# Performance work log

Hardware: AMD Instinct MI355X
Metric: run time of the kernel (lower is better)

The kernel has to match this reference:

```python
import jax, jax.numpy as jnp
import numpy as np

NUM_EMBEDDINGS = 512
EMBEDDING_DIM = 64
COMMITMENT_COST = 0.25


def setup_inputs() -> dict:
    key = jax.random.key(0)
    k1, k2 = jax.random.split(key)
    inputs = jax.random.normal(k1, (64, 32, 32, EMBEDDING_DIM), dtype=jnp.float32)
    # nn.Embedding weight init: uniform(-1/K, 1/K)
    codebook = jax.random.uniform(
        k2, (NUM_EMBEDDINGS, EMBEDDING_DIM), dtype=jnp.float32,
        minval=-1.0 / NUM_EMBEDDINGS, maxval=1.0 / NUM_EMBEDDINGS)
    return {"inputs": inputs, "codebook": codebook}


def reference(inputs, codebook):
    D = codebook.shape[1]
    K = codebook.shape[0]
    flat = inputs.reshape(-1, D)  # [N, D]
    # Squared euclidean distances (argmin-equivalent to torch.cdist output)
    d2 = (jnp.sum(flat * flat, axis=1, keepdims=True)
          - 2.0 * (flat @ codebook.T)
          + jnp.sum(codebook * codebook, axis=1))  # [N, K]
    idx = jnp.argmin(d2, axis=1)  # [N]
    # Gather codebook rows (== one-hot @ codebook in the original)
    quantized = codebook[idx].reshape(inputs.shape)
    e_latent_loss = jnp.mean((jax.lax.stop_gradient(quantized) - inputs) ** 2)
    q_latent_loss = jnp.mean((quantized - jax.lax.stop_gradient(inputs)) ** 2)
    loss = q_latent_loss + COMMITMENT_COST * e_latent_loss
    # Straight-through estimator
    quantized_st = inputs + jax.lax.stop_gradient(quantized - inputs)
    # Perplexity from code usage histogram (== mean of one-hot encodings)
    n = flat.shape[0]
    avg_probs = jnp.zeros((K,), dtype=jnp.float32).at[idx].add(1.0) / n
    perplexity = jnp.exp(-jnp.sum(avg_probs * jnp.log(avg_probs + 1e-10)))
    encoding_indices = idx[:, None]  # [N, 1] to match torch unsqueeze(1)
    return (loss, quantized_st, perplexity, encoding_indices)
```

## Files before the change

### kernel.cpp

```cpp
#include <hip/hip_runtime.h>
#include <math.h>

#define K_EMB 512
#define DIM 64
#define NVEC 65536
#define OUT_LOSS 0
#define OUT_Q 1
#define OUT_PERP (1 + NVEC * DIM)
#define OUT_IDX (1 + NVEC * DIM + 1)
#define EPS2 1e-4f
#define FIX_CAP 16

typedef __attribute__((ext_vector_type(8))) short short8;
typedef __attribute__((ext_vector_type(4))) float float4v;


__device__ __forceinline__ unsigned short bf16_rn(float f) {
    unsigned u = __float_as_uint(f);
    return (unsigned short)((u + 0x7FFFu + ((u >> 16) & 1u)) >> 16);
}

__device__ __forceinline__ float np_pairwise8_sq(const float* v) {
    float r[8];
#pragma unroll
    for (int j = 0; j < 8; ++j) r[j] = __fmul_rn(v[j], v[j]);
#pragma unroll
    for (int i = 8; i < 64; i += 8) {
#pragma unroll
        for (int j = 0; j < 8; ++j) r[j] = __fadd_rn(r[j], __fmul_rn(v[i + j], v[i + j]));
    }
    return __fadd_rn(__fadd_rn(__fadd_rn(r[0], r[1]), __fadd_rn(r[2], r[3])),
                     __fadd_rn(__fadd_rn(r[4], r[5]), __fadd_rn(r[6], r[7])));
}

__global__ void vq_frag(const float* __restrict__ codebook, float* __restrict__ csq,
                        unsigned short* __restrict__ ahi, unsigned short* __restrict__ alo,
                        float4* __restrict__ csqf, unsigned* __restrict__ hist,
                        double* __restrict__ sse64) {
    const int tid = threadIdx.x;
    if (blockIdx.x < 16) {
        const int id = blockIdx.x * 256 + tid;
        const int t = id >> 7, step = (id >> 6) & 1, lane = id & 63;
        const int m = t * 16 + (lane & 15);
        const int kb = step * 32 + (lane >> 4) * 8;
        const float4* src = (const float4*)(codebook + (m << 6) + kb);
        float4 f0 = src[0], f1 = src[1];
        const float fs[8] = {f0.x, f0.y, f0.z, f0.w, f1.x, f1.y, f1.z, f1.w};
        short8 h, l;
#pragma unroll
        for (int j = 0; j < 8; ++j) {
            unsigned short hv = bf16_rn(fs[j]);
            float lof = fs[j] - __uint_as_float(((unsigned)hv) << 16);
            h[j] = (short)hv;
            l[j] = (short)bf16_rn(lof);
        }
        const int fo = ((t * 2 + step) * 64 + lane) * 8;
        *(short8*)(ahi + fo) = h;
        *(short8*)(alo + fo) = l;
    } else {
        __shared__ float s_csq[512];
#pragma unroll
        for (int r = 0; r < 2; ++r) {
            const int k = tid + 256 * r;
            float v = np_pairwise8_sq(codebook + ((size_t)k << 6));
            s_csq[k] = v;
            csq[k] = v;
            hist[k] = 0u;
        }
        if (tid < 64) sse64[tid] = 0.0;
        __syncthreads();
#pragma unroll
        for (int i = 0; i < 8; ++i) {
            const int id = i * 256 + tid;
            const int t = id >> 6, lane = id & 63;
            const int k0 = t * 16 + (lane >> 4) * 4;
            csqf[id] = make_float4(s_csq[k0], s_csq[k0 + 1], s_csq[k0 + 2], s_csq[k0 + 3]);
        }
    }
}

__launch_bounds__(256, 4)
__global__ void vq_main(const float* __restrict__ inputs, const float* __restrict__ codebook,
                        const float* __restrict__ csq, const unsigned short* __restrict__ ahi,
                        const unsigned short* __restrict__ alo, const float4* __restrict__ csqf,
                        unsigned* __restrict__ hist, double* __restrict__ sse64,
                        float* __restrict__ out) {
    __shared__ __align__(16) float s_x[32 * 68];
    __shared__ float s_A[32];
    __shared__ unsigned long long s_t1[4][32];
    __shared__ unsigned long long s_t2[4][32];
    __shared__ unsigned long long s_e[32];
    __shared__ int s_fix[FIX_CAP];
    __shared__ int s_nfix;
    __shared__ float s_w[4];

    const int tid = threadIdx.x;
    const int wave = tid >> 6, lane = tid & 63;
    const int vbase = blockIdx.x * 32;

    if (tid == 0) s_nfix = 0;

    {
        const float4* src = (const float4*)(inputs + ((size_t)vbase << 6));
#pragma unroll
        for (int i = 0; i < 2; ++i) {
            const int f = i * 256 + tid;
            float4 v = src[f];
            *(float4*)&s_x[(f >> 4) * 68 + (f & 15) * 4] = v;
        }
    }
    __syncthreads();

    if (tid < 32) s_A[tid] = np_pairwise8_sq(&s_x[tid * 68]);
    __syncthreads();

    short8 bhi[2][2], blo[2][2];
#pragma unroll
    for (int vt = 0; vt < 2; ++vt) {
        const int vrow = vt * 16 + (lane & 15);
#pragma unroll
        for (int step = 0; step < 2; ++step) {
            const int kb = step * 32 + (lane >> 4) * 8;
            float4 f0 = *(const float4*)&s_x[vrow * 68 + kb];
            float4 f1 = *(const float4*)&s_x[vrow * 68 + kb + 4];
            const float fs[8] = {f0.x, f0.y, f0.z, f0.w, f1.x, f1.y, f1.z, f1.w};
            short8 h, l;
#pragma unroll
            for (int j = 0; j < 8; ++j) {
                unsigned short hv = bf16_rn(fs[j]);
                float lof = fs[j] - __uint_as_float(((unsigned)hv) << 16);
                h[j] = (short)hv;
                l[j] = (short)bf16_rn(lof);
            }
            bhi[vt][step] = h;
            blo[vt][step] = l;
        }
    }

    unsigned long long e1[2] = {~0ULL, ~0ULL}, e2[2] = {~0ULL, ~0ULL};

#pragma unroll 2
    for (int tt = 0; tt < 8; ++tt) {
        const int t = wave * 8 + tt;
        const int fo0 = ((t * 2 + 0) * 64 + lane) * 8;
        const int fo1 = ((t * 2 + 1) * 64 + lane) * 8;
        short8 ah0 = *(const short8*)(ahi + fo0);
        short8 ah1 = *(const short8*)(ahi + fo1);
        short8 al0 = *(const short8*)(alo + fo0);
        short8 al1 = *(const short8*)(alo + fo1);
        float4 cs = csqf[t * 64 + lane];
        const float csr[4] = {cs.x, cs.y, cs.z, cs.w};
#pragma unroll
        for (int vt = 0; vt < 2; ++vt) {
            float4v acc = {0.f, 0.f, 0.f, 0.f};
            acc = __builtin_amdgcn_mfma_f32_16x16x32_bf16(ah0, bhi[vt][0], acc, 0, 0, 0);
            acc = __builtin_amdgcn_mfma_f32_16x16x32_bf16(ah1, bhi[vt][1], acc, 0, 0, 0);
            acc = __builtin_amdgcn_mfma_f32_16x16x32_bf16(ah0, blo[vt][0], acc, 0, 0, 0);
            acc = __builtin_amdgcn_mfma_f32_16x16x32_bf16(ah1, blo[vt][1], acc, 0, 0, 0);
            acc = __builtin_amdgcn_mfma_f32_16x16x32_bf16(al0, bhi[vt][0], acc, 0, 0, 0);
            acc = __builtin_amdgcn_mfma_f32_16x16x32_bf16(al1, bhi[vt][1], acc, 0, 0, 0);
            const float Avt = s_A[vt * 16 + (lane & 15)];
#pragma unroll
            for (int r = 0; r < 4; ++r) {
                float d2 = __fadd_rn(__fsub_rn(Avt, __fmul_rn(2.0f, acc[r])), csr[r]);
                const unsigned k = (unsigned)(t * 16 + (lane >> 4) * 4 + r);
                unsigned long long e = ((unsigned long long)__float_as_uint(d2) << 32) | k;
                if (e < e1[vt]) { e2[vt] = e1[vt]; e1[vt] = e; }
                else if (e < e2[vt]) e2[vt] = e;
            }
        }
    }

#pragma unroll
    for (int vt = 0; vt < 2; ++vt) {
#pragma unroll
        for (int off = 16; off <= 32; off <<= 1) {
            unsigned long long o1 = __shfl_xor(e1[vt], off);
            unsigned long long o2 = __shfl_xor(e2[vt], off);
            if (o1 < e1[vt]) { e2[vt] = (e1[vt] < o2) ? e1[vt] : o2; e1[vt] = o1; }
            else if (o1 < e2[vt]) e2[vt] = o1;
        }
        if (lane < 16) {
            s_t1[wave][vt * 16 + lane] = e1[vt];
            s_t2[wave][vt * 16 + lane] = e2[vt];
        }
    }
    __syncthreads();

    if (tid < 32) {
        unsigned long long E1 = ~0ULL, E2 = ~0ULL;
#pragma unroll
        for (int w = 0; w < 4; ++w) {
            unsigned long long a = s_t1[w][tid], b = s_t2[w][tid];
            if (a < E1) { E2 = (E1 < b) ? E1 : b; E1 = a; }
            else if (a < E2) E2 = a;
        }
        s_e[tid] = E1;
        float b1 = __uint_as_float((unsigned)(E1 >> 32));
        float b2 = __uint_as_float((unsigned)(E2 >> 32));
        if (__fsub_rn(b2, b1) <= EPS2) {
            int pos = atomicAdd(&s_nfix, 1);
            if (pos < FIX_CAP) s_fix[pos] = tid;
        }
    }
    __syncthreads();

    {
        int nf = s_nfix; if (nf > FIX_CAP) nf = FIX_CAP;
        for (int f = wave; f < nf; f += 4) {
            const int vloc = s_fix[f];
            const float* xr = &s_x[vloc * 68];
            const float A = s_A[vloc];
            unsigned long long best = ~0ULL;
#pragma unroll 1
            for (int r8 = 0; r8 < 8; ++r8) {
                const int k = lane * 8 + r8;
                const float* c = codebook + (k << 6);
                float p[8] = {0.f, 0.f, 0.f, 0.f, 0.f, 0.f, 0.f, 0.f};
#pragma unroll
                for (int ii = 0; ii < 64; ii += 8)
#pragma unroll
                    for (int j = 0; j < 8; ++j)
                        p[j] = __builtin_fmaf(xr[ii + j], c[ii + j], p[j]);
                float dot = __fadd_rn(__fadd_rn(__fadd_rn(p[0], p[1]), __fadd_rn(p[2], p[3])),
                                      __fadd_rn(__fadd_rn(p[4], p[5]), __fadd_rn(p[6], p[7])));
                float d2 = __fadd_rn(__fsub_rn(A, __fmul_rn(2.0f, dot)), csq[k]);
                unsigned long long e = ((unsigned long long)__float_as_uint(d2) << 32) | (unsigned)k;
                if (e < best) best = e;
            }
#pragma unroll
            for (int off = 32; off > 0; off >>= 1) {
                unsigned long long o = __shfl_down(best, off);
                if (o < best) best = o;
            }
            if (lane == 0) s_e[vloc] = best;
        }
    }
    __syncthreads();

    if (tid < 32) {
        const unsigned kf = (unsigned)s_e[tid];
        out[OUT_IDX + vbase + tid] = (float)kf;
        atomicAdd(&hist[kf], 1u);
    }
    {
        float4* dst = (float4*)(out + OUT_Q + ((size_t)vbase << 6));
        float es = 0.f;
#pragma unroll
        for (int i = 0; i < 2; ++i) {
            const int f = i * 256 + tid;
            const int row = f >> 4, col = (f & 15) * 4;
            const unsigned k = (unsigned)s_e[row];
            float4 qv = *(const float4*)(codebook + ((size_t)k << 6) + col);
            dst[f] = qv;
            float4 xv = *(const float4*)&s_x[row * 68 + col];
            float d0 = qv.x - xv.x; es = __builtin_fmaf(d0, d0, es);
            float d1 = qv.y - xv.y; es = __builtin_fmaf(d1, d1, es);
            float d2 = qv.z - xv.z; es = __builtin_fmaf(d2, d2, es);
            float d3 = qv.w - xv.w; es = __builtin_fmaf(d3, d3, es);
        }
#pragma unroll
        for (int off = 32; off > 0; off >>= 1) es += __shfl_down(es, off);
        if (lane == 0) s_w[wave] = es;
    }
    __syncthreads();
    if (tid == 0)
        atomicAdd(&sse64[blockIdx.x & 63],
                  (double)(((s_w[0] + s_w[1]) + (s_w[2] + s_w[3]))));
}

__global__ void vq_final(const unsigned* __restrict__ hist, const double* __restrict__ sse64,
                         float* __restrict__ out) {
    __shared__ float s_wsm[8];
    const int k = threadIdx.x;
    float pr = (float)hist[k] / 65536.0f;
    float v = __fmul_rn(pr, logf(__fadd_rn(pr, 1e-10f)));
#pragma unroll
    for (int off = 32; off > 0; off >>= 1) v += __shfl_down(v, off);
    if ((k & 63) == 0) s_wsm[k >> 6] = v;
    __syncthreads();
    if (k == 0) {
        float S = 0.f;
#pragma unroll
        for (int i = 0; i < 8; ++i) S += s_wsm[i];
        out[OUT_PERP] = expf(-S);
        double sv = 0.0;
        for (int i = 0; i < 64; ++i) sv += sse64[i];
        float m = (float)(sv / 4194304.0);
        out[OUT_LOSS] = __fadd_rn(m, __fmul_rn(0.25f, m));
    }
}

extern "C" void kernel_launch(void* const* d_in, const int* in_sizes, int n_in,
                              void* d_out, int out_size, void* d_ws, size_t ws_size,
                              hipStream_t stream) {
    const float* inputs   = (const float*)d_in[0];
    const float* codebook = (const float*)d_in[1];
    float* out = (float*)d_out;
    float*          csq   = (float*)d_ws;
    double*         sse64 = (double*)((char*)d_ws + 2048);
    unsigned*       hist  = (unsigned*)((char*)d_ws + 2560);
    unsigned short* ahi   = (unsigned short*)((char*)d_ws + 4608);
    unsigned short* alo   = (unsigned short*)((char*)d_ws + 70144);
    float4*         csqf  = (float4*)((char*)d_ws + 135680);

    vq_frag<<<17, 256, 0, stream>>>(codebook, csq, ahi, alo, csqf, hist, sse64);
    vq_main<<<2048, 256, 0, stream>>>(inputs, codebook, csq, ahi, alo, csqf, hist, sse64, out);
    vq_final<<<1, 512, 0, stream>>>(hist, sse64, out);
}
```

Baseline: 136.8 us.

## Fuse final reduction into main kernel and parallelize input bf16 split

Removes the separate vq_final launch: the last block to finish, found through an atomic ticket counter, computes perplexity and loss. The input hi/lo bf16 split and the squared norms are now spread across all 256 threads through shared memory, where before 32 threads did the norms serially. It also rotates the codebook tile order per block to spread global load traffic, cuts the sse slots to 32, and vectorizes the codebook norm loads. In exchange it adds a threadfence plus an atomic counter per block, and the squared norm now uses a different summation order.

Measured after the change: 175.0 us. +27.9%, slower.

```diff
diff --git a/kernel.cpp b/kernel.cpp
--- a/kernel.cpp
+++ b/kernel.cpp
@@ -10,6 +10,8 @@
 #define OUT_IDX (1 + NVEC * DIM + 1)
 #define EPS2 1e-4f
 #define FIX_CAP 16
+#define GRID_MAIN 2048
+#define SSE_SLOTS 32
 
 typedef __attribute__((ext_vector_type(8))) short short8;
 typedef __attribute__((ext_vector_type(4))) float float4v;
@@ -33,10 +35,30 @@
                      __fadd_rn(__fadd_rn(r[4], r[5]), __fadd_rn(r[6], r[7])));
 }
 
+__device__ __forceinline__ float np_pairwise8_sq_g(const float* g) {
+    float x[64];
+    const float4* v4 = (const float4*)g;
+#pragma unroll
+    for (int i = 0; i < 16; ++i) {
+        float4 t = v4[i];
+        x[4 * i + 0] = t.x; x[4 * i + 1] = t.y; x[4 * i + 2] = t.z; x[4 * i + 3] = t.w;
+    }
+    float r[8];
+#pragma unroll
+    for (int j = 0; j < 8; ++j) r[j] = __fmul_rn(x[j], x[j]);
+#pragma unroll
+    for (int i = 8; i < 64; i += 8) {
+#pragma unroll
+        for (int j = 0; j < 8; ++j) r[j] = __fadd_rn(r[j], __fmul_rn(x[i + j], x[i + j]));
+    }
+    return __fadd_rn(__fadd_rn(__fadd_rn(r[0], r[1]), __fadd_rn(r[2], r[3])),
+                     __fadd_rn(__fadd_rn(r[4], r[5]), __fadd_rn(r[6], r[7])));
+}
+
 __global__ void vq_frag(const float* __restrict__ codebook, float* __restrict__ csq,
                         unsigned short* __restrict__ ahi, unsigned short* __restrict__ alo,
                         float4* __restrict__ csqf, unsigned* __restrict__ hist,
-                        double* __restrict__ sse64) {
+                        double* __restrict__ sse64, unsigned* __restrict__ cnt) {
     const int tid = threadIdx.x;
     if (blockIdx.x < 16) {
         const int id = blockIdx.x * 256 + tid;
@@ -62,12 +84,13 @@
 #pragma unroll
         for (int r = 0; r < 2; ++r) {
             const int k = tid + 256 * r;
-            float v = np_pairwise8_sq(codebook + ((size_t)k << 6));
+            float v = np_pairwise8_sq_g(codebook + ((size_t)k << 6));
             s_csq[k] = v;
             csq[k] = v;
             hist[k] = 0u;
         }
-        if (tid < 64) sse64[tid] = 0.0;
+        if (tid < SSE_SLOTS) sse64[tid] = 0.0;
+        if (tid == SSE_SLOTS) *cnt = 0u;
         __syncthreads();
 #pragma unroll
         for (int i = 0; i < 8; ++i) {
@@ -84,8 +107,10 @@
                         const float* __restrict__ csq, const unsigned short* __restrict__ ahi,
                         const unsigned short* __restrict__ alo, const float4* __restrict__ csqf,
                         unsigned* __restrict__ hist, double* __restrict__ sse64,
-                        float* __restrict__ out) {
+                        unsigned* __restrict__ cnt, float* __restrict__ out) {
     __shared__ __align__(16) float s_x[32 * 68];
+    __shared__ __align__(16) unsigned short s_bh[2][2][64][8];
+    __shared__ __align__(16) unsigned short s_bl[2][2][64][8];
     __shared__ float s_A[32];
     __shared__ unsigned long long s_t1[4][32];
     __shared__ unsigned long long s_t2[4][32];
@@ -93,6 +118,9 @@
     __shared__ int s_fix[FIX_CAP];
     __shared__ int s_nfix;
     __shared__ float s_w[4];
+    __shared__ int s_last;
+    __shared__ float s_wsm[8];
+    __shared__ double s_sse[SSE_SLOTS];
 
     const int tid = threadIdx.x;
     const int wave = tid >> 6, lane = tid & 63;
@@ -111,37 +139,47 @@
     }
     __syncthreads();
 
-    if (tid < 32) s_A[tid] = np_pairwise8_sq(&s_x[tid * 68]);
+    {
+        const int row = tid >> 3, kc = tid & 7;
+        const float* p = &s_x[row * 68 + kc * 8];
+        float4 f0 = *(const float4*)p;
+        float4 f1 = *(const float4*)(p + 4);
+        const float fs[8] = {f0.x, f0.y, f0.z, f0.w, f1.x, f1.y, f1.z, f1.w};
+        float s = 0.f;
+        short8 h, l;
+#pragma unroll
+        for (int j = 0; j < 8; ++j) {
+            s = __builtin_fmaf(fs[j], fs[j], s);
+            unsigned short hv = bf16_rn(fs[j]);
+            float lof = fs[j] - __uint_as_float(((unsigned)hv) << 16);
+            h[j] = (short)hv;
+            l[j] = (short)bf16_rn(lof);
+        }
+        const int vt = row >> 4, ln = ((kc & 3) << 4) | (row & 15), step = (kc >> 2) & 1;
+        *(short8*)&s_bh[vt][step][ln][0] = h;
+        *(short8*)&s_bl[vt][step][ln][0] = l;
+        s += __shfl_xor(s, 1);
+        s += __shfl_xor(s, 2);
+        s += __shfl_xor(s, 4);
+        if (kc == 0) s_A[row] = s;
+    }
     __syncthreads();
 
     short8 bhi[2][2], blo[2][2];
 #pragma unroll
-    for (int vt = 0; vt < 2; ++vt) {
-        const int vrow = vt * 16 + (lane & 15);
+    for (int vt = 0; vt < 2; ++vt)
 #pragma unroll
         for (int step = 0; step < 2; ++step) {
-            const int kb = step * 32 + (lane >> 4) * 8;
-            float4 f0 = *(const float4*)&s_x[vrow * 68 + kb];
-            float4 f1 = *(const float4*)&s_x[vrow * 68 + kb + 4];
-            const float fs[8] = {f0.x, f0.y, f0.z, f0.w, f1.x, f1.y, f1.z, f1.w};
-            short8 h, l;
-#pragma unroll
-            for (int j = 0; j < 8; ++j) {
-                unsigned short hv = bf16_rn(fs[j]);
-                float lof = fs[j] - __uint_as_float(((unsigned)hv) << 16);
-                h[j] = (short)hv;
-                l[j] = (short)bf16_rn(lof);
-            }
-            bhi[vt][step] = h;
-            blo[vt][step] = l;
-        }
-    }
+            bhi[vt][step] = *(const short8*)&s_bh[vt][step][lane][0];
+            blo[vt][step] = *(const short8*)&s_bl[vt][step][lane][0];
+        }
 
     unsigned long long e1[2] = {~0ULL, ~0ULL}, e2[2] = {~0ULL, ~0ULL};
+    const int rot = (int)((blockIdx.x >> 3) & 7);
 
 #pragma unroll 2
     for (int tt = 0; tt < 8; ++tt) {
-        const int t = wave * 8 + tt;
+        const int t = wave * 8 + ((tt + rot) & 7);
         const int fo0 = ((t * 2 + 0) * 64 + lane) * 8;
         const int fo1 = ((t * 2 + 1) * 64 + lane) * 8;
         short8 ah0 = *(const short8*)(ahi + fo0);
@@ -210,7 +248,7 @@
         for (int f = wave; f < nf; f += 4) {
             const int vloc = s_fix[f];
             const float* xr = &s_x[vloc * 68];
-            const float A = s_A[vloc];
+            const float A = np_pairwise8_sq(xr);
             unsigned long long best = ~0ULL;
 #pragma unroll 1
             for (int r8 = 0; r8 < 8; ++r8) {
@@ -264,30 +302,38 @@
         if (lane == 0) s_w[wave] = es;
     }
     __syncthreads();
-    if (tid == 0)
-        atomicAdd(&sse64[blockIdx.x & 63],
+    if (tid == 0) {
+        atomicAdd(&sse64[blockIdx.x & (SSE_SLOTS - 1)],
                   (double)(((s_w[0] + s_w[1]) + (s_w[2] + s_w[3]))));
-}
-
-__global__ void vq_final(const unsigned* __restrict__ hist, const double* __restrict__ sse64,
-                         float* __restrict__ out) {
-    __shared__ float s_wsm[8];
-    const int k = threadIdx.x;
-    float pr = (float)hist[k] / 65536.0f;
-    float v = __fmul_rn(pr, logf(__fadd_rn(pr, 1e-10f)));
-#pragma unroll
-    for (int off = 32; off > 0; off >>= 1) v += __shfl_down(v, off);
-    if ((k & 63) == 0) s_wsm[k >> 6] = v;
-    __syncthreads();
-    if (k == 0) {
-        float S = 0.f;
-#pragma unroll
-        for (int i = 0; i < 8; ++i) S += s_wsm[i];
-        out[OUT_PERP] = expf(-S);
-        double sv = 0.0;
-        for (int i = 0; i < 64; ++i) sv += sse64[i];
-        float m = (float)(sv / 4194304.0);
-        out[OUT_LOSS] = __fadd_rn(m, __fmul_rn(0.25f, m));
+        __threadfence();
+        unsigned ticket = atomicAdd(cnt, 1u);
+        s_last = (ticket == GRID_MAIN - 1) ? 1 : 0;
+    }
+    __syncthreads();
+
+    if (s_last) {
+        float pr0 = (float)atomicAdd(&hist[tid], 0u) / 65536.0f;
+        float v0 = __fmul_rn(pr0, logf(__fadd_rn(pr0, 1e-10f)));
+        float pr1 = (float)atomicAdd(&hist[tid + 256], 0u) / 65536.0f;
+        float v1 = __fmul_rn(pr1, logf(__fadd_rn(pr1, 1e-10f)));
+#pragma unroll
+        for (int off = 32; off > 0; off >>= 1) {
+            v0 += __shfl_down(v0, off);
+            v1 += __shfl_down(v1, off);
+        }
+        if (lane == 0) { s_wsm[wave] = v0; s_wsm[4 + wave] = v1; }
+        if (tid < SSE_SLOTS) s_sse[tid] = atomicAdd(&sse64[tid], 0.0);
+        __syncthreads();
+        if (tid == 0) {
+            float S = 0.f;
+#pragma unroll
+            for (int i = 0; i < 8; ++i) S += s_wsm[i];
+            out[OUT_PERP] = expf(-S);
+            double sv = 0.0;
+            for (int i = 0; i < SSE_SLOTS; ++i) sv += s_sse[i];
+            float m = (float)(sv / 4194304.0);
+            out[OUT_LOSS] = __fadd_rn(m, __fmul_rn(0.25f, m));
+        }
     }
 }
 
@@ -299,12 +345,12 @@
     float* out = (float*)d_out;
     float*          csq   = (float*)d_ws;
     double*         sse64 = (double*)((char*)d_ws + 2048);
+    unsigned*       cnt   = (unsigned*)((char*)d_ws + 2304);
     unsigned*       hist  = (unsigned*)((char*)d_ws + 2560);
     unsigned short* ahi   = (unsigned short*)((char*)d_ws + 4608);
     unsigned short* alo   = (unsigned short*)((char*)d_ws + 70144);
     float4*         csqf  = (float4*)((char*)d_ws + 135680);
 
-    vq_frag<<<17, 256, 0, stream>>>(codebook, csq, ahi, alo, csqf, hist, sse64);
-    vq_main<<<2048, 256, 0, stream>>>(inputs, codebook, csq, ahi, alo, csqf, hist, sse64, out);
-    vq_final<<<1, 512, 0, stream>>>(hist, sse64, out);
-}
+    vq_frag<<<17, 256, 0, stream>>>(codebook, csq, ahi, alo, csqf, hist, sse64, cnt);
+    vq_main<<<GRID_MAIN, 256, 0, stream>>>(inputs, codebook, csq, ahi, alo, csqf, hist, sse64, cnt, out);
+}
```
